# Performance work log

Hardware: AMD Instinct MI355X
Metric: run time of the kernel (lower is better)

## Reference

```python
import jax, jax.numpy as jnp
import numpy as np

# ---- geometry constants (from init_kwargs) ----
VOL_SHAPE = (96, 96, 96)        # (Z, Y, X)
VOL_SPACING = 1.0               # mm, isotropic
N_PROJ = 180
DET_ROWS, DET_COLS = 192, 384   # (v, u)
DET_SPACING_V, DET_SPACING_U = 1.0, 1.0
SID = 750.0                     # source-isocenter distance
SDD = 1200.0                    # source-detector distance


def _proj_matrices():
    """3x4 pinhole projection matrices for a circular cone-beam trajectory."""
    cu = (DET_COLS - 1) / 2.0
    cv = (DET_ROWS - 1) / 2.0
    Kc = np.array([[SDD / DET_SPACING_U, 0.0, cu],
                   [0.0, SDD / DET_SPACING_V, cv],
                   [0.0, 0.0, 1.0]])
    mats = []
    for th in np.linspace(0.0, 2.0 * np.pi, N_PROJ, endpoint=False):
        s = SID * np.array([np.cos(th), np.sin(th), 0.0])   # source position
        ez = -s / SID                                        # optical axis -> isocenter
        ex = np.array([-np.sin(th), np.cos(th), 0.0])        # detector u axis
        ey = np.array([0.0, 0.0, 1.0])                       # detector v axis
        R = np.stack([ex, ey, ez])                           # world -> camera
        P = Kc @ np.concatenate([R, (-R @ s)[:, None]], axis=1)
        mats.append(P)
    return np.stack(mats).astype(np.float32)                # [P, 3, 4]


def _voxel_coords():
    """Homogeneous world coordinates of all voxel centers, [4, N]."""
    zs = (np.arange(VOL_SHAPE[0]) - (VOL_SHAPE[0] - 1) / 2.0) * VOL_SPACING
    ys = (np.arange(VOL_SHAPE[1]) - (VOL_SHAPE[1] - 1) / 2.0) * VOL_SPACING
    xs = (np.arange(VOL_SHAPE[2]) - (VOL_SHAPE[2] - 1) / 2.0) * VOL_SPACING
    Z, Y, X = np.meshgrid(zs, ys, xs, indexing='ij')
    pts = np.stack([X.ravel(), Y.ravel(), Z.ravel(), np.ones(X.size)])
    return pts.astype(np.float32)


def _bilinear(img, u, v):
    """Zero-padded bilinear interpolation of img[H,W] at (v,u) pixel coords."""
    H, W = img.shape
    u0 = jnp.floor(u); v0 = jnp.floor(v)
    fu = u - u0; fv = v - v0
    u0i = u0.astype(jnp.int32); v0i = v0.astype(jnp.int32)
    def at(vi, ui):
        valid = (ui >= 0) & (ui < W) & (vi >= 0) & (vi < H)
        val = img[jnp.clip(vi, 0, H - 1), jnp.clip(ui, 0, W - 1)]
        return jnp.where(valid, val, jnp.zeros((), img.dtype))
    return (at(v0i, u0i) * (1 - fu) * (1 - fv)
            + at(v0i, u0i + 1) * fu * (1 - fv)
            + at(v0i + 1, u0i) * (1 - fu) * fv
            + at(v0i + 1, u0i + 1) * fu * fv)


def _backproject_one(sino, mats, coords):
    """sino [P,H,W], mats [P,3,4], coords [4,N] -> volume [Z,Y,X]."""
    N = coords.shape[1]
    @jax.checkpoint
    def step(acc, pm_s):
        P, s = pm_s
        uvw = P @ coords                      # [3, N]
        w = uvw[2]                            # ray depth along optical axis (>0)
        u = uvw[0] / w
        v = uvw[1] / w
        acc = acc + _bilinear(s, u, v) / (w * w)  # FDK distance weighting
        return acc, None
    acc, _ = jax.lax.scan(step, jnp.zeros((N,), sino.dtype), (mats, sino))
    return acc.reshape(VOL_SHAPE)


def setup_inputs() -> dict:
    key = jax.random.key(0)
    x = jax.random.normal(key, (2, N_PROJ, DET_ROWS, DET_COLS, 1), dtype=jnp.float32)
    proj_matrices = jnp.asarray(_proj_matrices())
    return {"x": x, "proj_matrices": proj_matrices}


def reference(x, proj_matrices):
    coords = jnp.asarray(_voxel_coords())                 # [4, N]
    sinos = jnp.squeeze(x, -1)                            # [B, P, H, W]
    vols = jax.vmap(lambda s: _backproject_one(s, proj_matrices, coords))(sinos)
    return vols[..., None]                                # [B, Z, Y, X, 1]
```

## Files before the change

kernel.cpp:

```cpp
#include <hip/hip_runtime.h>

#define NPROJ 180
#define DH 192
#define DW 384
#define VN 96
#define ZPER 8
#define ZCH (VN / ZPER)
#define TCOLS 65
#define TROWS 19
#define TSTG 1280
#define PSTRIDE (DH * DW)
#define BSTRIDE (NPROJ * DH * DW)

typedef float v2f __attribute__((ext_vector_type(2)));

template<int PQ, int NQ>
__global__ __launch_bounds__(256, 6) void cone_bp(
    const float* __restrict__ sino,
    const float* __restrict__ mats,
    float* __restrict__ out,
    float* __restrict__ ws)
{
    __shared__ v2f tile[2][TSTG];
    __shared__ int2 anch[PQ];

    const int tid = threadIdx.x;
    const int x = blockIdx.x * 32 + ((tid & 7) | ((tid >> 6) << 3));
    const int y = blockIdx.y * 8 + ((tid >> 3) & 7);
    const int zc = blockIdx.z % ZCH;
    const int qt = blockIdx.z / ZCH;
    const int pbase = qt * PQ;

    const float xw = (float)x - 47.5f;
    const float yw = (float)y - 47.5f;
    const float zw0 = (float)(zc * ZPER) - 47.5f;

    const float xwc = (float)(blockIdx.x * 32) - 32.0f;
    const float ywc = (float)(blockIdx.y * 8) - 44.0f;
    const float zwc = (float)(zc * ZPER) - 44.0f;

    const float4* __restrict__ M = (const float4*)mats;

    if (tid < PQ) {
        int p = pbase + tid;
        float4 a0 = M[p * 3 + 0];
        float4 a1 = M[p * 3 + 1];
        float4 a2 = M[p * 3 + 2];
        float unc = fmaf(a0.x, xwc, fmaf(a0.y, ywc, a0.w));
        float vnc = fmaf(a1.x, xwc, fmaf(a1.y, ywc, fmaf(a1.z, zwc, a1.w)));
        float wc  = fmaf(a2.x, xwc, fmaf(a2.y, ywc, a2.w));
        float rwc = __builtin_amdgcn_rcpf(wc);
        anch[tid] = make_int2((int)floorf(unc * rwc) - 31,
                              (int)floorf(vnc * rwc) - 9);
    }

    int VgB[5];
#pragma unroll
    for (int k = 0; k < 5; ++k) {
        int li = tid + 256 * k;
        int row = li / TCOLS;
        int col = li - row * TCOLS;
        VgB[k] = (row * DW + col) * 4;
    }

    __syncthreads();

    int cu, cv;
    {
        int2 a = anch[0];
        cu = __builtin_amdgcn_readfirstlane(a.x);
        cv = __builtin_amdgcn_readfirstlane(a.y);
    }
    v2f g[5];
    {
        const char* p0 = (const char*)(sino + pbase * PSTRIDE + cv * DW + cu);
        const char* p1 = p0 + (size_t)BSTRIDE * 4;
#pragma unroll
        for (int k = 0; k < 5; ++k) {
            g[k].x = *(const float*)(p0 + VgB[k]);
            g[k].y = *(const float*)(p1 + VgB[k]);
        }
    }

    v2f acc[ZPER];
#pragma unroll
    for (int k = 0; k < ZPER; ++k) acc[k] = (v2f)(0.0f);

    auto body = [&](int i, v2f* __restrict__ buf) {
#pragma unroll
        for (int k = 0; k < 5; ++k)
            buf[tid + 256 * k] = g[k];
        const float nfu = -(float)cu;
        const float nfv = -(float)cv;

        if (i + 1 < PQ) {
            int2 a = anch[i + 1];
            cu = __builtin_amdgcn_readfirstlane(a.x);
            cv = __builtin_amdgcn_readfirstlane(a.y);
            const char* p0 = (const char*)(sino
                + (pbase + i + 1) * PSTRIDE + cv * DW + cu);
            const char* p1 = p0 + (size_t)BSTRIDE * 4;
#pragma unroll
            for (int k = 0; k < 5; ++k) {
                g[k].x = *(const float*)(p0 + VgB[k]);
                g[k].y = *(const float*)(p1 + VgB[k]);
            }
        }

        __syncthreads();

        const int p = pbase + i;
        float4 r0 = M[p * 3 + 0];
        float4 r1 = M[p * 3 + 1];
        float4 r2 = M[p * 3 + 2];
        float un  = fmaf(r0.x, xw, fmaf(r0.y, yw, r0.w));
        float vn0 = fmaf(r1.x, xw, fmaf(r1.y, yw, r1.w));
        float w   = fmaf(r2.x, xw, fmaf(r2.y, yw, r2.w));
        float rw  = __builtin_amdgcn_rcpf(w);
        float iw2 = rw * rw;
        float ul  = fmaf(un, rw, nfu);
        float uf  = floorf(ul);
        float fu  = ul - uf;
        int   u0l = (int)uf;
        float vb  = fmaf(fmaf(r1.z, zw0, vn0), rw, nfv);
        float dv  = r1.z * rw;

#pragma unroll
        for (int gz = 0; gz < 2; ++gz) {
            int   o[4];
            float fv[4];
#pragma unroll
            for (int j = 0; j < 4; ++j) {
                float v  = fmaf(dv, (float)(4 * gz + j), vb);
                float vf = floorf(v);
                fv[j] = v - vf;
                o[j] = (int)vf * TCOLS + u0l;
            }
            v2f E00[4], E01[4], E10[4], E11[4];
#pragma unroll
            for (int j = 0; j < 4; ++j) {
                E00[j] = buf[o[j]];
                E01[j] = buf[o[j] + 1];
                E10[j] = buf[o[j] + TCOLS];
                E11[j] = buf[o[j] + TCOLS + 1];
            }
#pragma unroll
            for (int j = 0; j < 4; ++j) {
                v2f F0 = E00[j] + (E10[j] - E00[j]) * fv[j];
                v2f F1 = E01[j] + (E11[j] - E01[j]) * fv[j];
                v2f H  = F0 + (F1 - F0) * fu;
                acc[4 * gz + j] += H * iw2;
            }
        }
    };

    for (int i = 0; i < PQ; i += 2) {
        body(i, tile[0]);
        if (i + 1 < PQ) body(i + 1, tile[1]);
    }

    float* __restrict__ dst = (NQ == 4 && qt >= 2) ? ws : out;
    const int zbase = zc * ZPER;
#pragma unroll
    for (int k = 0; k < ZPER; ++k) {
        unsafeAtomicAdd(&dst[(((size_t)(zbase + k)) * VN + y) * VN + x],
                        acc[k].x);
        unsafeAtomicAdd(&dst[(((size_t)(VN + zbase + k)) * VN + y) * VN + x],
                        acc[k].y);
    }
}

__global__ __launch_bounds__(256) void add_ws(
    float4* __restrict__ out, const float4* __restrict__ ws, int n4)
{
    int i = blockIdx.x * 256 + threadIdx.x;
    if (i < n4) {
        float4 a = ws[i];
        float4 b = out[i];
        b.x += a.x; b.y += a.y; b.z += a.z; b.w += a.w;
        out[i] = b;
    }
}

extern "C" void kernel_launch(void* const* d_in, const int* in_sizes, int n_in,
                              void* d_out, int out_size, void* d_ws, size_t ws_size,
                              hipStream_t stream) {
    const float* sino = (const float*)d_in[0];
    const float* mats = (const float*)d_in[1];
    float* out = (float*)d_out;
    float* wsf = (float*)d_ws;

    const size_t nvox = (size_t)2 * VN * VN * VN;
    hipMemsetAsync(out, 0, (size_t)out_size * sizeof(float), stream);

    if (ws_size >= nvox * sizeof(float)) {
        hipMemsetAsync(wsf, 0, nvox * sizeof(float), stream);
        dim3 grid(VN / 32, VN / 8, ZCH * 4), block(256);
        hipLaunchKernelGGL((cone_bp<NPROJ / 4, 4>), grid, block, 0, stream,
                           sino, mats, out, wsf);
        int n4 = (int)(nvox / 4);
        hipLaunchKernelGGL(add_ws, dim3((n4 + 255) / 256), block, 0, stream,
                           (float4*)out, (const float4*)wsf, n4);
    } else {
        dim3 grid(VN / 32, VN / 8, ZCH * 2), block(256);
        hipLaunchKernelGGL((cone_bp<NPROJ / 2, 2>), grid, block, 0, stream,
                           sino, mats, out, (float*)nullptr);
    }
}
```

Baseline: 311.4 us.

## Give each wavefront its own detector tile to drop block-wide barriers

Each 64-lane wavefront now handles its own 8x8 voxel column over its own z-chunk. It stages a private 20x16 double-buffered detector tile in LDS, so the per-projection __syncthreads is no longer needed. Projection anchors are kept in registers and fetched with readlane rather than through shared memory, and occupancy launch bounds are raised to 8. The risk is that the smaller per-wave tile may not cover the projected footprint at oblique angles. The stores and loads also rely on implicit wavefront-level ordering with no barrier.

```diff
diff --git a/kernel.cpp b/kernel.cpp
--- a/kernel.cpp
+++ b/kernel.cpp
@@ -6,43 +6,47 @@
 #define VN 96
 #define ZPER 8
 #define ZCH (VN / ZPER)
-#define TCOLS 65
-#define TROWS 19
-#define TSTG 1280
+#define TCOLS 20
+#define TROWS 16
+#define TENT (TCOLS * TROWS)
 #define PSTRIDE (DH * DW)
 #define BSTRIDE (NPROJ * DH * DW)
 
 typedef float v2f __attribute__((ext_vector_type(2)));
 
 template<int PQ, int NQ>
-__global__ __launch_bounds__(256, 6) void cone_bp(
+__global__ __launch_bounds__(256, 8) void cone_bp(
     const float* __restrict__ sino,
     const float* __restrict__ mats,
     float* __restrict__ out,
     float* __restrict__ ws)
 {
-    __shared__ v2f tile[2][TSTG];
-    __shared__ int2 anch[PQ];
-
-    const int tid = threadIdx.x;
-    const int x = blockIdx.x * 32 + ((tid & 7) | ((tid >> 6) << 3));
-    const int y = blockIdx.y * 8 + ((tid >> 3) & 7);
-    const int zc = blockIdx.z % ZCH;
-    const int qt = blockIdx.z / ZCH;
+    __shared__ v2f tile[4][2][TENT];
+
+    const int tid  = threadIdx.x;
+    const int lane = tid & 63;
+    const int wv   = tid >> 6;
+
+    const int lx = lane & 7;
+    const int ly = lane >> 3;
+    const int zi = blockIdx.z % 3;
+    const int qt = blockIdx.z / 3;
+    const int zch = zi * 4 + wv;
     const int pbase = qt * PQ;
 
+    const int x = blockIdx.x * 8 + lx;
+    const int y = blockIdx.y * 8 + ly;
     const float xw = (float)x - 47.5f;
     const float yw = (float)y - 47.5f;
-    const float zw0 = (float)(zc * ZPER) - 47.5f;
-
-    const float xwc = (float)(blockIdx.x * 32) - 32.0f;
+    const float zw0 = (float)(zch * ZPER) - 47.5f;
+
+    const float xwc = (float)(blockIdx.x * 8) - 44.0f;
     const float ywc = (float)(blockIdx.y * 8) - 44.0f;
-    const float zwc = (float)(zc * ZPER) - 44.0f;
+    const float zwc = (float)(zch * ZPER) - 44.0f;
 
     const float4* __restrict__ M = (const float4*)mats;
 
-    if (tid < PQ) {
-        int p = pbase + tid;
+    auto anchor = [&](int p) -> int {
         float4 a0 = M[p * 3 + 0];
         float4 a1 = M[p * 3 + 1];
         float4 a2 = M[p * 3 + 2];
@@ -50,65 +54,59 @@
         float vnc = fmaf(a1.x, xwc, fmaf(a1.y, ywc, fmaf(a1.z, zwc, a1.w)));
         float wc  = fmaf(a2.x, xwc, fmaf(a2.y, ywc, a2.w));
         float rwc = __builtin_amdgcn_rcpf(wc);
-        anch[tid] = make_int2((int)floorf(unc * rwc) - 31,
-                              (int)floorf(vnc * rwc) - 9);
-    }
-
-    int VgB[5];
+        int iu0 = (int)floorf(unc * rwc) - 9;
+        int iv0 = (int)floorf(vnc * rwc) - 7;
+        return iu0 | (iv0 << 16);
+    };
+    int au = anchor(pbase + (lane < PQ ? lane : PQ - 1));
+    int av = 0;
+    if constexpr (PQ > 64)
+        av = anchor(pbase + (lane + 64 < PQ ? lane + 64 : PQ - 1));
+
+    auto getAnchor = [&](int idx, int& cu, int& cv) {
+        int a;
+        if constexpr (PQ > 64)
+            a = (idx < 64) ? __builtin_amdgcn_readlane(au, idx)
+                           : __builtin_amdgcn_readlane(av, idx - 64);
+        else
+            a = __builtin_amdgcn_readlane(au, idx);
+        cu = a & 0xffff;
+        cv = a >> 16;
+    };
+
+    int Vg[5];
 #pragma unroll
     for (int k = 0; k < 5; ++k) {
-        int li = tid + 256 * k;
+        int li = lane + 64 * k;
         int row = li / TCOLS;
         int col = li - row * TCOLS;
-        VgB[k] = (row * DW + col) * 4;
-    }
-
-    __syncthreads();
-
-    int cu, cv;
-    {
-        int2 a = anch[0];
-        cu = __builtin_amdgcn_readfirstlane(a.x);
-        cv = __builtin_amdgcn_readfirstlane(a.y);
-    }
+        Vg[k] = row * DW + col;
+    }
+
     v2f g[5];
-    {
-        const char* p0 = (const char*)(sino + pbase * PSTRIDE + cv * DW + cu);
-        const char* p1 = p0 + (size_t)BSTRIDE * 4;
+    auto issue = [&](int p, int cu, int cv) {
+        const float* __restrict__ base =
+            sino + ((size_t)p * PSTRIDE + cv * DW + cu);
 #pragma unroll
         for (int k = 0; k < 5; ++k) {
-            g[k].x = *(const float*)(p0 + VgB[k]);
-            g[k].y = *(const float*)(p1 + VgB[k]);
+            g[k].x = base[Vg[k]];
+            g[k].y = base[Vg[k] + BSTRIDE];
         }
-    }
+    };
+
+    v2f* const buf0 = tile[wv][0];
+    v2f* const buf1 = tile[wv][1];
+    auto store = [&](v2f* buf) {
+#pragma unroll
+        for (int k = 0; k < 5; ++k)
+            buf[lane + 64 * k] = g[k];
+    };
 
     v2f acc[ZPER];
 #pragma unroll
     for (int k = 0; k < ZPER; ++k) acc[k] = (v2f)(0.0f);
 
-    auto body = [&](int i, v2f* __restrict__ buf) {
-#pragma unroll
-        for (int k = 0; k < 5; ++k)
-            buf[tid + 256 * k] = g[k];
-        const float nfu = -(float)cu;
-        const float nfv = -(float)cv;
-
-        if (i + 1 < PQ) {
-            int2 a = anch[i + 1];
-            cu = __builtin_amdgcn_readfirstlane(a.x);
-            cv = __builtin_amdgcn_readfirstlane(a.y);
-            const char* p0 = (const char*)(sino
-                + (pbase + i + 1) * PSTRIDE + cv * DW + cu);
-            const char* p1 = p0 + (size_t)BSTRIDE * 4;
-#pragma unroll
-            for (int k = 0; k < 5; ++k) {
-                g[k].x = *(const float*)(p0 + VgB[k]);
-                g[k].y = *(const float*)(p1 + VgB[k]);
-            }
-        }
-
-        __syncthreads();
-
+    auto sample = [&](int i, const v2f* buf, float nfu, float nfv) {
         const int p = pbase + i;
         float4 r0 = M[p * 3 + 0];
         float4 r1 = M[p * 3 + 1];
@@ -124,7 +122,6 @@
         int   u0l = (int)uf;
         float vb  = fmaf(fmaf(r1.z, zw0, vn0), rw, nfv);
         float dv  = r1.z * rw;
-
 #pragma unroll
         for (int gz = 0; gz < 2; ++gz) {
             int   o[4];
@@ -154,13 +151,43 @@
         }
     };
 
+    int cu, cv;
+    getAnchor(0, cu, cv);
+    issue(pbase, cu, cv);
+    float nfu0 = -(float)cu, nfv0 = -(float)cv;
+    store(buf0);
+    float nfuC = 0.0f, nfvC = 0.0f;
+    if (PQ > 1) {
+        getAnchor(1, cu, cv);
+        issue(pbase + 1, cu, cv);
+        nfuC = -(float)cu; nfvC = -(float)cv;
+    }
+
     for (int i = 0; i < PQ; i += 2) {
-        body(i, tile[0]);
-        if (i + 1 < PQ) body(i + 1, tile[1]);
+        sample(i, buf0, nfu0, nfv0);
+        if (i + 1 < PQ) {
+            store(buf1);
+            float nfu1 = nfuC, nfv1 = nfvC;
+            if (i + 2 < PQ) {
+                getAnchor(i + 2, cu, cv);
+                issue(pbase + i + 2, cu, cv);
+                nfuC = -(float)cu; nfvC = -(float)cv;
+            }
+            sample(i + 1, buf1, nfu1, nfv1);
+            if (i + 2 < PQ) {
+                store(buf0);
+                nfu0 = nfuC; nfv0 = nfvC;
+                if (i + 3 < PQ) {
+                    getAnchor(i + 3, cu, cv);
+                    issue(pbase + i + 3, cu, cv);
+                    nfuC = -(float)cu; nfvC = -(float)cv;
+                }
+            }
+        }
     }
 
     float* __restrict__ dst = (NQ == 4 && qt >= 2) ? ws : out;
-    const int zbase = zc * ZPER;
+    const int zbase = zch * ZPER;
 #pragma unroll
     for (int k = 0; k < ZPER; ++k) {
         unsafeAtomicAdd(&dst[(((size_t)(zbase + k)) * VN + y) * VN + x],
@@ -195,14 +222,14 @@
 
     if (ws_size >= nvox * sizeof(float)) {
         hipMemsetAsync(wsf, 0, nvox * sizeof(float), stream);
-        dim3 grid(VN / 32, VN / 8, ZCH * 4), block(256);
+        dim3 grid(VN / 8, VN / 8, 3 * 4), block(256);
         hipLaunchKernelGGL((cone_bp<NPROJ / 4, 4>), grid, block, 0, stream,
                            sino, mats, out, wsf);
         int n4 = (int)(nvox / 4);
         hipLaunchKernelGGL(add_ws, dim3((n4 + 255) / 256), block, 0, stream,
                            (float4*)out, (const float4*)wsf, n4);
     } else {
-        dim3 grid(VN / 32, VN / 8, ZCH * 2), block(256);
+        dim3 grid(VN / 8, VN / 8, 3 * 2), block(256);
         hipLaunchKernelGGL((cone_bp<NPROJ / 2, 2>), grid, block, 0, stream,
                            sino, mats, out, (float*)nullptr);
     }
```

Result: slower. 1.179 ms (+278.7%).
